# Performance work log

Measured on AMD Instinct MI355X. Metric: run time of the kernel, lower is better.

The kernel has to match this reference:

```python
import jax, jax.numpy as jnp
import numpy as np

NUM_CLASSES = 22
CLIP_LENGTH = 256.0
OVERLAP_THRESH = 0.5
EPS = 1.1920929e-07  # torch.finfo(float32).eps
BOUNDS_LO = jnp.array([0., 15., 30., 60., 96., 256.], dtype=jnp.float32)
BOUNDS_HI = jnp.array([30., 60., 120., 240., 768., 768.], dtype=jnp.float32)


def setup_inputs() -> dict:
    key = jax.random.key(0)
    ks = jax.random.split(key, 9)
    B, K, C, N = 8, 100000, NUM_CLASSES, 32
    loc_data = jax.random.uniform(ks[0], (B, K, 2), jnp.float32)
    conf_data = jax.random.normal(ks[1], (B, K, C), jnp.float32)
    prop_loc_data = jax.random.uniform(ks[2], (B, K, 2), jnp.float32)
    prop_conf_data = jax.random.normal(ks[3], (B, K, C), jnp.float32)
    center_data = jax.random.normal(ks[4], (B, K, 1), jnp.float32)
    # priors: [K,2] = (center in [0,1], pyramid-level index 0..5)
    centers = (jnp.arange(K, dtype=jnp.float32) + 0.5) / K
    levels = jax.random.randint(ks[5], (K,), 0, 6).astype(jnp.float32)
    priors = jnp.stack([centers, levels], axis=-1)
    # targets: [B,N,3] = (start, end, label), label in 1..C-1
    starts = jax.random.uniform(ks[6], (B, N), jnp.float32, 0.0, 0.8)
    lens = jax.random.uniform(ks[7], (B, N), jnp.float32, 0.02, 0.3)
    ends = jnp.clip(starts + lens, 0.0, 1.0)
    labels = jax.random.randint(ks[8], (B, N), 1, C).astype(jnp.float32)
    targets = jnp.stack([starts, ends, labels], axis=-1)
    return {"loc_data": loc_data, "conf_data": conf_data,
            "prop_loc_data": prop_loc_data, "prop_conf_data": prop_conf_data,
            "center_data": center_data, "priors": priors, "targets": targets}


def _calc_iou(pred, tgt):
    # pred/tgt: [..., 2] = (left, right) distances; 1-D segment IoU
    inter = jnp.minimum(pred[..., 0], tgt[..., 0]) + jnp.minimum(pred[..., 1], tgt[..., 1])
    union = pred[..., 0] + pred[..., 1] + tgt[..., 0] + tgt[..., 1] - inter
    return inter / jnp.maximum(union, EPS)


def _giou_elem(pred, tgt):
    inter = jnp.minimum(pred[..., 0], tgt[..., 0]) + jnp.minimum(pred[..., 1], tgt[..., 1])
    union = pred[..., 0] + pred[..., 1] + tgt[..., 0] + tgt[..., 1] - inter
    ious = inter / jnp.maximum(union, EPS)
    ac = jnp.maximum(pred[..., 0], tgt[..., 0]) + jnp.maximum(pred[..., 1], tgt[..., 1])
    gious = ious - (ac - union) / jnp.maximum(ac, EPS)
    return 1.0 - gious


def _focal_sum(logits, tgt):
    # FocalLoss_Ori: softmax probs, pt = p[target]+1e-10, alpha[0]=0.25, alpha[1:]=0.75,
    # loss = -alpha_t * (1-pt)^2 * log(pt), summed over anchors -> [B]
    probs = jax.nn.softmax(logits, axis=-1)
    pt = jnp.take_along_axis(probs, tgt[..., None], axis=-1)[..., 0] + 1e-10
    alpha_t = jnp.where(tgt == 0, 0.25, 0.75)
    return (-alpha_t * (1.0 - pt) ** 2 * jnp.log(pt)).sum(axis=1)


def _forward(loc_data, conf_data, prop_loc_data, prop_conf_data, center_data, priors, targets):
    B, K, C = conf_data.shape
    maxn = 2.0 * CLIP_LENGTH

    def match():  # torch.no_grad() block
        center = priors[:, 0]                              # [K]
        lvl = priors[:, 1].astype(jnp.int32)
        lb = BOUNDS_LO[lvl][None, :, None]                 # [1,K,1]
        rb = BOUNDS_HI[lvl][None, :, None]
        ts, te = targets[..., 0], targets[..., 1]          # [B,N]
        left = (center[None, :, None] - ts[:, None, :]) * CLIP_LENGTH   # [B,K,N]
        right = (te[:, None, :] - center[None, :, None]) * CLIP_LENGTH
        max_dis = jnp.maximum(left, right)
        area = left + right
        bad = (left < 0) | (right < 0) | (max_dis <= lb) | (max_dis > rb)
        area = jnp.where(bad, maxn, area)
        best_area = area.min(axis=2)                       # [B,K]
        best_idx = area.argmin(axis=2)                     # [B,K]
        gs = jnp.take_along_axis(ts, best_idx, axis=1)
        ge = jnp.take_along_axis(te, best_idx, axis=1)
        loc_t = jnp.stack([(center[None, :] - gs) * CLIP_LENGTH,
                           (ge - center[None, :]) * CLIP_LENGTH], axis=-1)  # [B,K,2]
        labels = targets[..., 2]
        conf = jnp.take_along_axis(labels, best_idx, axis=1).astype(jnp.int32)
        conf = jnp.where(best_area >= maxn, 0, conf)
        iou = _calc_iou(loc_data, loc_t)                   # [B,K]
        pos = conf > 0
        has_pos = pos.any(axis=1)
        max_iou = jnp.where(has_pos, jnp.where(pos, iou, -jnp.inf).max(axis=1), 2.0)
        thr = jnp.minimum(OVERLAP_THRESH, max_iou)[:, None]
        prop_conf = jnp.where(iou < thr, 0, conf)
        prop_w = loc_data[..., 0] + loc_data[..., 1]
        prop_loc_t = (loc_t - loc_data) / (0.5 * prop_w[..., None])
        return loc_t, conf, prop_conf, prop_loc_t

    loc_t, conf_t, prop_conf_t, prop_loc_t = jax.lax.stop_gradient(match())
    pos = conf_t > 0                                       # [B,K]
    prop_pos = prop_conf_t > 0
    Nb = jnp.maximum(pos.sum(axis=1), 1).astype(jnp.float32)
    PNb = jnp.maximum(prop_pos.sum(axis=1), 1).astype(jnp.float32)

    # loc giou loss over positives
    loss_l = jnp.where(pos, _giou_elem(loc_data, loc_t), 0.0).sum(axis=1) / Nb

    # prop smooth_l1 over prop positives (beta=1)
    d = jnp.abs(prop_loc_data - prop_loc_t)
    sl1 = jnp.where(d < 1.0, 0.5 * d * d, d - 0.5).sum(axis=-1)   # [B,K]
    loss_prop_l = jnp.where(prop_pos, sl1, 0.0).sum(axis=1) / PNb

    # centerness BCE-with-logits vs refined IoU over positives
    prop_w = loc_data[..., 0] + loc_data[..., 1]
    cur_loc_p = 0.5 * prop_w[..., None] * prop_loc_data + loc_data
    ious_c = jnp.maximum(_calc_iou(cur_loc_p, loc_t), 0.0)
    x = center_data[..., 0]
    bce = jax.nn.softplus(x) - x * ious_c                  # BCEWithLogits(x, y)
    loss_ct = jnp.where(pos, bce, 0.0).sum(axis=1) / Nb

    # focal classification losses over ALL anchors
    loss_c = _focal_sum(conf_data, conf_t) / Nb
    loss_prop_c = _focal_sum(prop_conf_data, prop_conf_t) / PNb

    return jnp.stack([loss_l.mean(), loss_c.mean(), loss_prop_l.mean(),
                      loss_prop_c.mean(), loss_ct.mean()])


def reference(loc_data, conf_data, prop_loc_data, prop_conf_data, center_data, priors, targets):
    return _forward(loc_data, conf_data, prop_loc_data, prop_conf_data,
                    center_data, priors, targets)
```

## Files before the change

kernel.cpp:

```cpp
#include <hip/hip_runtime.h>
#include <math.h>
#include <stdint.h>

#define BLK 256
#define NCLS 22
#define ROWB 88
#define WROWS 32
#define CHB (WROWS * ROWB)
#define CH2 (CHB / 8)
#define EPSF 1.1920929e-07f
#define K1CHUNK (BLK * 4)
#define NB1MAX 128

__device__ __constant__ float c_lo[6] = {0.f, 15.f, 30.f, 60.f, 96.f, 256.f};
__device__ __constant__ float c_hi[6] = {30.f, 60.f, 120.f, 240.f, 768.f, 768.f};

struct MatchRes { float t0, t1; int conf; };

template <int NN>
__device__ __forceinline__ MatchRes do_match_u(float center, int lvl, const float* tg) {
    float lb = c_lo[lvl], rb = c_hi[lvl];
    float best = 1e30f; int bidx = 0;
#pragma unroll
    for (int j = 0; j < NN; ++j) {
        float ts = tg[3 * j], te = tg[3 * j + 1];
        float left  = (center - ts) * 256.f;
        float right = (te - center) * 256.f;
        float md   = fmaxf(left, right);
        float area = left + right;
        bool bad = (left < 0.f) | (right < 0.f) | (md <= lb) | (md > rb);
        area = bad ? 512.f : area;
        if (area < best) { best = area; bidx = j; }
    }
    MatchRes r;
    float gs = tg[3 * bidx], ge = tg[3 * bidx + 1];
    r.t0 = (center - gs) * 256.f;
    r.t1 = (ge - center) * 256.f;
    r.conf = (best >= 512.f) ? 0 : (int)tg[3 * bidx + 2];
    return r;
}

__device__ __forceinline__ MatchRes do_match_d(float center, int lvl, const float* tg, int N) {
    float lb = c_lo[lvl], rb = c_hi[lvl];
    float best = 1e30f; int bidx = 0;
    for (int j = 0; j < N; ++j) {
        float ts = tg[3 * j], te = tg[3 * j + 1];
        float left  = (center - ts) * 256.f;
        float right = (te - center) * 256.f;
        float md   = fmaxf(left, right);
        float area = left + right;
        bool bad = (left < 0.f) | (right < 0.f) | (md <= lb) | (md > rb);
        area = bad ? 512.f : area;
        if (area < best) { best = area; bidx = j; }
    }
    MatchRes r;
    float gs = tg[3 * bidx], ge = tg[3 * bidx + 1];
    r.t0 = (center - gs) * 256.f;
    r.t1 = (ge - center) * 256.f;
    r.conf = (best >= 512.f) ? 0 : (int)tg[3 * bidx + 2];
    return r;
}

__device__ __forceinline__ float calc_iou(float px, float py, float t0, float t1) {
    float inter = fminf(px, t0) + fminf(py, t1);
    float uni = px + py + t0 + t1 - inter;
    return inter / fmaxf(uni, EPSF);
}

__device__ __forceinline__ float focal22_lds(const float2* r2, int tgt) {
    float v[NCLS];
#pragma unroll
    for (int i = 0; i < NCLS / 2; ++i) { float2 x = r2[i]; v[2 * i] = x.x; v[2 * i + 1] = x.y; }
    float m0 = v[0], m1 = v[1], m2 = v[2], m3 = v[3];
#pragma unroll
    for (int i = 4; i < NCLS; i += 4) {
        m0 = fmaxf(m0, v[i]);
        m1 = fmaxf(m1, v[i + 1]);
        if (i + 2 < NCLS) m2 = fmaxf(m2, v[i + 2]);
        if (i + 3 < NCLS) m3 = fmaxf(m3, v[i + 3]);
    }
    float m = fmaxf(fmaxf(m0, m1), fmaxf(m2, m3));
    float sA = 0.f, sB = 0.f, eA = 0.f, eB = 0.f;
#pragma unroll
    for (int i = 0; i < NCLS; i += 2) {
        float ea = __expf(v[i] - m);
        float eb = __expf(v[i + 1] - m);
        sA += ea; sB += eb;
        eA += (i == tgt) ? ea : 0.f;
        eB += (i + 1 == tgt) ? eb : 0.f;
    }
    float pt = (eA + eB) / (sA + sB) + 1e-10f;
    float aa = (tgt == 0) ? 0.25f : 0.75f;
    float om = 1.f - pt;
    return -aa * om * om * __logf(pt);
}

__global__ __launch_bounds__(BLK) void k1_match(const float* __restrict__ loc,
                                                const float* __restrict__ priors,
                                                const float* __restrict__ targets,
                                                float* __restrict__ wsmax,
                                                int K, int N) {
    int b = blockIdx.y;
    __shared__ float tg[96];
    __shared__ float red[4];
    if (threadIdx.x < 3 * N) tg[threadIdx.x] = targets[b * 3 * N + threadIdx.x];
    __syncthreads();
    float my = -INFINITY;
    for (int base = blockIdx.x * K1CHUNK; base < K; base += gridDim.x * K1CHUNK) {
        for (int it = 0; it < 2; ++it) {
            int k0 = base + it * (BLK * 2) + threadIdx.x * 2;
            if (k0 < K) {
                size_t idx = (size_t)b * K + k0;
                float4 pr = reinterpret_cast<const float4*>(priors)[k0 >> 1];
                float4 lp = reinterpret_cast<const float4*>(loc)[idx >> 1];
                MatchRes r0 = (N == 32) ? do_match_u<32>(pr.x, (int)pr.y, tg)
                                        : do_match_d(pr.x, (int)pr.y, tg, N);
                MatchRes r1 = (N == 32) ? do_match_u<32>(pr.z, (int)pr.w, tg)
                                        : do_match_d(pr.z, (int)pr.w, tg, N);
                if (r0.conf > 0) my = fmaxf(my, calc_iou(lp.x, lp.y, r0.t0, r0.t1));
                if (((k0 + 1) < K) && r1.conf > 0)
                    my = fmaxf(my, calc_iou(lp.z, lp.w, r1.t0, r1.t1));
            }
        }
    }
#pragma unroll
    for (int off = 32; off; off >>= 1) my = fmaxf(my, __shfl_xor(my, off));
    int wid = threadIdx.x >> 6;
    if ((threadIdx.x & 63) == 0) red[wid] = my;
    __syncthreads();
    if (threadIdx.x == 0)
        wsmax[b * gridDim.x + blockIdx.x] =
            fmaxf(fmaxf(red[0], red[1]), fmaxf(red[2], red[3]));
}

template <bool UN32>
__global__ __launch_bounds__(BLK) void k2_loss(const float* __restrict__ loc,
                                               const float* __restrict__ conf,
                                               const float* __restrict__ ploc,
                                               const float* __restrict__ pconf,
                                               const float* __restrict__ cent,
                                               const float* __restrict__ priors,
                                               const float* __restrict__ targets,
                                               const float* __restrict__ wsmax,
                                               float* __restrict__ wspart,
                                               int K, int N, int nb1) {
    int b = blockIdx.y;
    int wid = threadIdx.x >> 6, lane = threadIdx.x & 63;
    __shared__ float tg[96];
    __shared__ float red[7][4];
    __shared__ __align__(16) float2 stage[4][2 * CH2];
    if (threadIdx.x < 3 * N) tg[threadIdx.x] = targets[b * 3 * N + threadIdx.x];
    __syncthreads();

    int rb = blockIdx.x * (4 * WROWS) + wid * WROWS;
    int rloc = lane >> 1;
    int r = rb + rloc;
    bool odd = lane & 1;
    bool act = r < K;
    int rc = act ? r : (K - 1);
    size_t idx = (size_t)b * K + rc;

    const float* xybase = odd ? ploc : loc;
    float2 xy = reinterpret_cast<const float2*>(xybase)[idx];
    float ccv = cent[idx];
    float2 pr = reinterpret_cast<const float2*>(priors)[rc];
    float w0 = (lane < nb1) ? wsmax[b * nb1 + lane] : -INFINITY;
    float w1 = (lane + 64 < nb1) ? wsmax[b * nb1 + lane + 64] : -INFINITY;

    float4 cr[3], qr[3];
    {
        const uint8_t* cg = (const uint8_t*)conf;
        const uint8_t* qg = (const uint8_t*)pconf;
        size_t cbase = ((size_t)b * K + (size_t)(rb < K ? rb : 0)) * ROWB;
        size_t endB = ((size_t)(b + 1) * K) * ROWB - 16;
#pragma unroll
        for (int i = 0; i < 3; ++i) {
            size_t so = cbase + (size_t)i * 1024 + (size_t)lane * 16;
            if (so > endB) so = endB;
            cr[i] = *reinterpret_cast<const float4*>(cg + so);
        }
#pragma unroll
        for (int i = 0; i < 3; ++i) {
            size_t so = cbase + (size_t)i * 1024 + (size_t)lane * 16;
            if (so > endB) so = endB;
            qr[i] = *reinterpret_cast<const float4*>(qg + so);
        }
    }

    float mx = fmaxf(w0, w1);
#pragma unroll
    for (int off = 32; off; off >>= 1) mx = fmaxf(mx, __shfl_xor(mx, off));
    float thr = (mx == -INFINITY) ? 0.5f : fminf(0.5f, mx);

    MatchRes mr = UN32 ? do_match_u<32>(pr.x, (int)pr.y, tg)
                       : do_match_d(pr.x, (int)pr.y, tg, N);
    int cf = mr.conf;
    float t0 = mr.t0, t1 = mr.t1;

    float ox = __shfl_xor(xy.x, 1), oy = __shfl_xor(xy.y, 1);
    float lpx = odd ? ox : xy.x, lpy = odd ? oy : xy.y;
    float ppx = odd ? xy.x : ox, ppy = odd ? xy.y : oy;

    float iou = calc_iou(lpx, lpy, t0, t1);
    int pc = (iou < thr) ? 0 : cf;
    float pw = lpx + lpy;

    float s_giou = 0.f, s_sl1 = 0.f, s_bce = 0.f, c_pos = 0.f, c_ppos = 0.f;
    if (!odd && act && cf > 0) {
        c_pos = 1.f;
        float inter = fminf(lpx, t0) + fminf(lpy, t1);
        float uni = lpx + lpy + t0 + t1 - inter;
        float ac = fmaxf(lpx, t0) + fmaxf(lpy, t1);
        float g = iou - (ac - uni) / fmaxf(ac, EPSF);
        s_giou = 1.f - g;
        float cl0 = 0.5f * pw * ppx + lpx;
        float cl1 = 0.5f * pw * ppy + lpy;
        float i2 = fminf(cl0, t0) + fminf(cl1, t1);
        float u2 = cl0 + cl1 + t0 + t1 - i2;
        float iouc = fmaxf(i2 / fmaxf(u2, EPSF), 0.f);
        float sp = fmaxf(ccv, 0.f) + log1pf(__expf(-fabsf(ccv)));
        s_bce = sp - ccv * iouc;
    }
    if (odd && act && pc > 0) {
        c_ppos = 1.f;
        float hpw = 0.5f * pw;
        float plt0 = (t0 - lpx) / hpw;
        float plt1 = (t1 - lpy) / hpw;
        float d0 = fabsf(ppx - plt0), d1 = fabsf(ppy - plt1);
        float f0 = (d0 < 1.f) ? 0.5f * d0 * d0 : d0 - 0.5f;
        float f1 = (d1 < 1.f) ? 0.5f * d1 * d1 : d1 - 0.5f;
        s_sl1 = f0 + f1;
    }

    {
        float2* sb = stage[wid];
#pragma unroll
        for (int i = 0; i < 3; ++i) {
            int e2 = i * 128 + lane * 2;
            if (e2 < CH2) {
                sb[e2]     = make_float2(cr[i].x, cr[i].y);
                sb[e2 + 1] = make_float2(cr[i].z, cr[i].w);
            }
        }
#pragma unroll
        for (int i = 0; i < 3; ++i) {
            int e2 = i * 128 + lane * 2;
            if (e2 < CH2) {
                sb[CH2 + e2]     = make_float2(qr[i].x, qr[i].y);
                sb[CH2 + e2 + 1] = make_float2(qr[i].z, qr[i].w);
            }
        }
    }
    asm volatile("s_waitcnt lgkmcnt(0)" ::: "memory");

    const float2* rowp = stage[wid] + (odd ? CH2 : 0) + rloc * (ROWB / 8);
    int ftgt = odd ? pc : cf;
    float f = act ? focal22_lds(rowp, ftgt) : 0.f;
    float s_fc  = odd ? 0.f : f;
    float s_fpc = odd ? f : 0.f;

#pragma unroll
    for (int off = 32; off; off >>= 1) {
        s_giou += __shfl_xor(s_giou, off);
        s_sl1  += __shfl_xor(s_sl1, off);
        s_bce  += __shfl_xor(s_bce, off);
        s_fc   += __shfl_xor(s_fc, off);
        s_fpc  += __shfl_xor(s_fpc, off);
        c_pos  += __shfl_xor(c_pos, off);
        c_ppos += __shfl_xor(c_ppos, off);
    }
    if ((threadIdx.x & 63) == 0) {
        red[0][wid] = s_giou; red[1][wid] = s_sl1; red[2][wid] = s_bce;
        red[3][wid] = s_fc;   red[4][wid] = s_fpc; red[5][wid] = c_pos;
        red[6][wid] = c_ppos;
    }
    __syncthreads();
    if (threadIdx.x < 7) {
        float v = red[threadIdx.x][0] + red[threadIdx.x][1] +
                  red[threadIdx.x][2] + red[threadIdx.x][3];
        wspart[((size_t)b * gridDim.x + blockIdx.x) * 8 + threadIdx.x] = v;
    }
}

__global__ __launch_bounds__(512) void k3_final(const float* __restrict__ wspart,
                                                float* __restrict__ out, int B, int nb2) {
    int w = threadIdx.x >> 6, lane = threadIdx.x & 63;
    __shared__ float ls[8][5];
    float s[7] = {0.f, 0.f, 0.f, 0.f, 0.f, 0.f, 0.f};
    if (w < B) {
        for (int e = lane; e < nb2; e += 64) {
            const float* a = wspart + ((size_t)w * nb2 + e) * 8;
#pragma unroll
            for (int i = 0; i < 7; ++i) s[i] += a[i];
        }
    }
#pragma unroll
    for (int off = 32; off; off >>= 1)
#pragma unroll
        for (int i = 0; i < 7; ++i) s[i] += __shfl_xor(s[i], off);
    if (w < B && lane == 0) {
        float Nb  = fmaxf(s[5], 1.f);
        float PNb = fmaxf(s[6], 1.f);
        ls[w][0] = s[0] / Nb;
        ls[w][1] = s[3] / Nb;
        ls[w][2] = s[1] / PNb;
        ls[w][3] = s[4] / PNb;
        ls[w][4] = s[2] / Nb;
    }
    __syncthreads();
    if (threadIdx.x < 5) {
        float tt = 0.f;
        for (int bb = 0; bb < B; ++bb) tt += ls[bb][threadIdx.x];
        out[threadIdx.x] = tt / (float)B;
    }
}

extern "C" void kernel_launch(void* const* d_in, const int* in_sizes, int n_in,
                              void* d_out, int out_size, void* d_ws, size_t ws_size,
                              hipStream_t stream) {
    const float* loc     = (const float*)d_in[0];
    const float* conf    = (const float*)d_in[1];
    const float* ploc    = (const float*)d_in[2];
    const float* pconf   = (const float*)d_in[3];
    const float* cent    = (const float*)d_in[4];
    const float* priors  = (const float*)d_in[5];
    const float* targets = (const float*)d_in[6];
    int K = in_sizes[5] / 2;
    int B = in_sizes[0] / (2 * K);
    int N = in_sizes[6] / (3 * B);

    float* wsmax  = (float*)d_ws;
    float* wspart = (float*)d_ws + 1024;
    float* out = (float*)d_out;

    int nb1 = (K + K1CHUNK - 1) / K1CHUNK;
    if (nb1 > NB1MAX) nb1 = NB1MAX;
    int rows_per_blk = 4 * WROWS;
    int nb2 = (K + rows_per_blk - 1) / rows_per_blk;

    k1_match<<<dim3(nb1, B), dim3(BLK), 0, stream>>>(loc, priors, targets, wsmax, K, N);
    if (N == 32)
        k2_loss<true><<<dim3(nb2, B), dim3(BLK), 0, stream>>>(
            loc, conf, ploc, pconf, cent, priors, targets, wsmax, wspart, K, N, nb1);
    else
        k2_loss<false><<<dim3(nb2, B), dim3(BLK), 0, stream>>>(
            loc, conf, ploc, pconf, cent, priors, targets, wsmax, wspart, K, N, nb1);
    k3_final<<<dim3(1), dim3(512), 0, stream>>>(wspart, out, B, nb2);
}
```

Before: 66.99 us.

## Process four row chunks per wave with double-buffered conf loads and lane-dense matching

```diff
diff --git a/kernel.cpp b/kernel.cpp
--- a/kernel.cpp
+++ b/kernel.cpp
@@ -6,8 +6,10 @@
 #define NCLS 22
 #define ROWB 88
 #define WROWS 32
-#define CHB (WROWS * ROWB)
-#define CH2 (CHB / 8)
+#define CPW 4
+#define RPW (WROWS * CPW)
+#define RPB (RPW * 4)
+#define CH2 352
 #define EPSF 1.1920929e-07f
 #define K1CHUNK (BLK * 4)
 #define NB1MAX 128
@@ -67,29 +69,27 @@
     return inter / fmaxf(uni, EPSF);
 }
 
+__device__ __forceinline__ float fmax3(float a, float b, float c) {
+    return fmaxf(fmaxf(a, b), c);
+}
+
 __device__ __forceinline__ float focal22_lds(const float2* r2, int tgt) {
     float v[NCLS];
 #pragma unroll
     for (int i = 0; i < NCLS / 2; ++i) { float2 x = r2[i]; v[2 * i] = x.x; v[2 * i + 1] = x.y; }
-    float m0 = v[0], m1 = v[1], m2 = v[2], m3 = v[3];
-#pragma unroll
-    for (int i = 4; i < NCLS; i += 4) {
-        m0 = fmaxf(m0, v[i]);
-        m1 = fmaxf(m1, v[i + 1]);
-        if (i + 2 < NCLS) m2 = fmaxf(m2, v[i + 2]);
-        if (i + 3 < NCLS) m3 = fmaxf(m3, v[i + 3]);
-    }
-    float m = fmaxf(fmaxf(m0, m1), fmaxf(m2, m3));
-    float sA = 0.f, sB = 0.f, eA = 0.f, eB = 0.f;
+    float xt = reinterpret_cast<const float*>(r2)[tgt];
+    float a0 = fmax3(v[0], v[1], v[2]),  a1 = fmax3(v[3], v[4], v[5]);
+    float a2 = fmax3(v[6], v[7], v[8]),  a3 = fmax3(v[9], v[10], v[11]);
+    float a4 = fmax3(v[12], v[13], v[14]), a5 = fmax3(v[15], v[16], v[17]);
+    float a6 = fmax3(v[18], v[19], v[20]);
+    float m = fmax3(fmax3(a0, a1, a2), fmax3(a3, a4, a5), fmaxf(a6, v[21]));
+    float sA = 0.f, sB = 0.f;
 #pragma unroll
     for (int i = 0; i < NCLS; i += 2) {
-        float ea = __expf(v[i] - m);
-        float eb = __expf(v[i + 1] - m);
-        sA += ea; sB += eb;
-        eA += (i == tgt) ? ea : 0.f;
-        eB += (i + 1 == tgt) ? eb : 0.f;
-    }
-    float pt = (eA + eB) / (sA + sB) + 1e-10f;
+        sA += __expf(v[i] - m);
+        sB += __expf(v[i + 1] - m);
+    }
+    float pt = __expf(xt - m) / (sA + sB) + 1e-10f;
     float aa = (tgt == 0) ? 0.25f : 0.75f;
     float om = 1.f - pt;
     return -aa * om * om * __logf(pt);
@@ -149,115 +149,130 @@
     __shared__ float tg[96];
     __shared__ float red[7][4];
     __shared__ __align__(16) float2 stage[4][2 * CH2];
+    __shared__ float2 msct[4][RPW];
+    __shared__ float  mscf[4][RPW];
     if (threadIdx.x < 3 * N) tg[threadIdx.x] = targets[b * 3 * N + threadIdx.x];
     __syncthreads();
 
-    int rb = blockIdx.x * (4 * WROWS) + wid * WROWS;
+    int rb = blockIdx.x * RPB + wid * RPW;
+    bool odd = lane & 1;
     int rloc = lane >> 1;
-    int r = rb + rloc;
-    bool odd = lane & 1;
-    bool act = r < K;
-    int rc = act ? r : (K - 1);
-    size_t idx = (size_t)b * K + rc;
-
-    const float* xybase = odd ? ploc : loc;
-    float2 xy = reinterpret_cast<const float2*>(xybase)[idx];
-    float ccv = cent[idx];
-    float2 pr = reinterpret_cast<const float2*>(priors)[rc];
+
     float w0 = (lane < nb1) ? wsmax[b * nb1 + lane] : -INFINITY;
     float w1 = (lane + 64 < nb1) ? wsmax[b * nb1 + lane + 64] : -INFINITY;
-
-    float4 cr[3], qr[3];
-    {
-        const uint8_t* cg = (const uint8_t*)conf;
-        const uint8_t* qg = (const uint8_t*)pconf;
-        size_t cbase = ((size_t)b * K + (size_t)(rb < K ? rb : 0)) * ROWB;
-        size_t endB = ((size_t)(b + 1) * K) * ROWB - 16;
-#pragma unroll
-        for (int i = 0; i < 3; ++i) {
-            size_t so = cbase + (size_t)i * 1024 + (size_t)lane * 16;
-            if (so > endB) so = endB;
-            cr[i] = *reinterpret_cast<const float4*>(cg + so);
-        }
-#pragma unroll
-        for (int i = 0; i < 3; ++i) {
-            size_t so = cbase + (size_t)i * 1024 + (size_t)lane * 16;
-            if (so > endB) so = endB;
-            qr[i] = *reinterpret_cast<const float4*>(qg + so);
-        }
-    }
-
     float mx = fmaxf(w0, w1);
 #pragma unroll
     for (int off = 32; off; off >>= 1) mx = fmaxf(mx, __shfl_xor(mx, off));
     float thr = (mx == -INFINITY) ? 0.5f : fminf(0.5f, mx);
 
-    MatchRes mr = UN32 ? do_match_u<32>(pr.x, (int)pr.y, tg)
-                       : do_match_d(pr.x, (int)pr.y, tg, N);
-    int cf = mr.conf;
-    float t0 = mr.t0, t1 = mr.t1;
-
-    float ox = __shfl_xor(xy.x, 1), oy = __shfl_xor(xy.y, 1);
-    float lpx = odd ? ox : xy.x, lpy = odd ? oy : xy.y;
-    float ppx = odd ? xy.x : ox, ppy = odd ? xy.y : oy;
-
-    float iou = calc_iou(lpx, lpy, t0, t1);
-    int pc = (iou < thr) ? 0 : cf;
-    float pw = lpx + lpy;
-
-    float s_giou = 0.f, s_sl1 = 0.f, s_bce = 0.f, c_pos = 0.f, c_ppos = 0.f;
-    if (!odd && act && cf > 0) {
-        c_pos = 1.f;
-        float inter = fminf(lpx, t0) + fminf(lpy, t1);
-        float uni = lpx + lpy + t0 + t1 - inter;
-        float ac = fmaxf(lpx, t0) + fmaxf(lpy, t1);
-        float g = iou - (ac - uni) / fmaxf(ac, EPSF);
-        s_giou = 1.f - g;
-        float cl0 = 0.5f * pw * ppx + lpx;
-        float cl1 = 0.5f * pw * ppy + lpy;
-        float i2 = fminf(cl0, t0) + fminf(cl1, t1);
-        float u2 = cl0 + cl1 + t0 + t1 - i2;
-        float iouc = fmaxf(i2 / fmaxf(u2, EPSF), 0.f);
-        float sp = fmaxf(ccv, 0.f) + log1pf(__expf(-fabsf(ccv)));
-        s_bce = sp - ccv * iouc;
-    }
-    if (odd && act && pc > 0) {
-        c_ppos = 1.f;
-        float hpw = 0.5f * pw;
-        float plt0 = (t0 - lpx) / hpw;
-        float plt1 = (t1 - lpy) / hpw;
-        float d0 = fabsf(ppx - plt0), d1 = fabsf(ppy - plt1);
-        float f0 = (d0 < 1.f) ? 0.5f * d0 * d0 : d0 - 0.5f;
-        float f1 = (d1 < 1.f) ? 0.5f * d1 * d1 : d1 - 0.5f;
-        s_sl1 = f0 + f1;
-    }
-
-    {
-        float2* sb = stage[wid];
-#pragma unroll
-        for (int i = 0; i < 3; ++i) {
-            int e2 = i * 128 + lane * 2;
-            if (e2 < CH2) {
-                sb[e2]     = make_float2(cr[i].x, cr[i].y);
-                sb[e2 + 1] = make_float2(cr[i].z, cr[i].w);
-            }
+#pragma unroll
+    for (int h = 0; h < 2; ++h) {
+        int r = rb + h * 64 + lane;
+        int rc = (r < K) ? r : (K - 1);
+        float2 pr = reinterpret_cast<const float2*>(priors)[rc];
+        MatchRes mr = UN32 ? do_match_u<32>(pr.x, (int)pr.y, tg)
+                           : do_match_d(pr.x, (int)pr.y, tg, N);
+        msct[wid][h * 64 + lane] = make_float2(mr.t0, mr.t1);
+        mscf[wid][h * 64 + lane] = (float)mr.conf;
+    }
+
+    const uint8_t* cg = (const uint8_t*)conf;
+    const uint8_t* qg = (const uint8_t*)pconf;
+    size_t endB = ((size_t)(b + 1) * K) * ROWB - 16;
+
+    float4 cA[3], qA[3], cB[3], qB[3];
+#define LOADC(c, cd, qd) {                                                        \
+    size_t cb = ((size_t)b * K + (size_t)(rb + (c) * WROWS)) * ROWB;              \
+    _Pragma("unroll") for (int i = 0; i < 3; ++i) {                               \
+        size_t so = cb + (size_t)i * 1024 + (size_t)lane * 16;                    \
+        if (so > endB) so = endB;                                                 \
+        cd[i] = *reinterpret_cast<const float4*>(cg + so); }                      \
+    _Pragma("unroll") for (int i = 0; i < 3; ++i) {                               \
+        size_t so = cb + (size_t)i * 1024 + (size_t)lane * 16;                    \
+        if (so > endB) so = endB;                                                 \
+        qd[i] = *reinterpret_cast<const float4*>(qg + so); } }
+
+#define STOREC(cd, qd) {                                                          \
+    float2* sb = stage[wid];                                                      \
+    _Pragma("unroll") for (int i = 0; i < 3; ++i) {                               \
+        int e2 = i * 128 + lane * 2;                                              \
+        if (e2 < CH2) {                                                           \
+            sb[e2]     = make_float2(cd[i].x, cd[i].y);                           \
+            sb[e2 + 1] = make_float2(cd[i].z, cd[i].w); } }                       \
+    _Pragma("unroll") for (int i = 0; i < 3; ++i) {                               \
+        int e2 = i * 128 + lane * 2;                                              \
+        if (e2 < CH2) {                                                           \
+            sb[CH2 + e2]     = make_float2(qd[i].x, qd[i].y);                     \
+            sb[CH2 + e2 + 1] = make_float2(qd[i].z, qd[i].w); } } }
+
+    LOADC(0, cA, qA)
+
+    float s_giou = 0.f, s_sl1 = 0.f, s_bce = 0.f, s_fc = 0.f, s_fpc = 0.f,
+          c_pos = 0.f, c_ppos = 0.f;
+
+#pragma unroll
+    for (int c = 0; c < CPW; ++c) {
+        if (c == 0)      { LOADC(1, cB, qB) }
+        else if (c == 1) { LOADC(2, cA, qA) }
+        else if (c == 2) { LOADC(3, cB, qB) }
+
+        int rl = c * WROWS + rloc;
+        int r = rb + rl;
+        bool act = r < K;
+        int rc = act ? r : (K - 1);
+        size_t idx = (size_t)b * K + rc;
+        const float* xyb = odd ? ploc : loc;
+        float2 xy = reinterpret_cast<const float2*>(xyb)[idx];
+        float ccv = odd ? 0.f : cent[idx];
+
+        if (c & 1) { STOREC(cB, qB) } else { STOREC(cA, qA) }
+        asm volatile("s_waitcnt lgkmcnt(0)" ::: "memory");
+
+        float2 mt = msct[wid][rl];
+        int cf = (int)mscf[wid][rl];
+        float t0 = mt.x, t1 = mt.y;
+
+        float ox = __shfl_xor(xy.x, 1), oy = __shfl_xor(xy.y, 1);
+        float lpx = odd ? ox : xy.x, lpy = odd ? oy : xy.y;
+        float ppx = odd ? xy.x : ox, ppy = odd ? xy.y : oy;
+
+        float iou = calc_iou(lpx, lpy, t0, t1);
+        int pc = (iou < thr) ? 0 : cf;
+        float pw = lpx + lpy;
+
+        if (!odd && act && cf > 0) {
+            c_pos += 1.f;
+            float inter = fminf(lpx, t0) + fminf(lpy, t1);
+            float uni = lpx + lpy + t0 + t1 - inter;
+            float ac = fmaxf(lpx, t0) + fmaxf(lpy, t1);
+            float g = iou - (ac - uni) / fmaxf(ac, EPSF);
+            s_giou += 1.f - g;
+            float cl0 = 0.5f * pw * ppx + lpx;
+            float cl1 = 0.5f * pw * ppy + lpy;
+            float i2 = fminf(cl0, t0) + fminf(cl1, t1);
+            float u2 = cl0 + cl1 + t0 + t1 - i2;
+            float iouc = fmaxf(i2 / fmaxf(u2, EPSF), 0.f);
+            float sp = fmaxf(ccv, 0.f) + log1pf(__expf(-fabsf(ccv)));
+            s_bce += sp - ccv * iouc;
         }
-#pragma unroll
-        for (int i = 0; i < 3; ++i) {
-            int e2 = i * 128 + lane * 2;
-            if (e2 < CH2) {
-                sb[CH2 + e2]     = make_float2(qr[i].x, qr[i].y);
-                sb[CH2 + e2 + 1] = make_float2(qr[i].z, qr[i].w);
-            }
+        if (odd && act && pc > 0) {
+            c_ppos += 1.f;
+            float hpw = 0.5f * pw;
+            float plt0 = (t0 - lpx) / hpw;
+            float plt1 = (t1 - lpy) / hpw;
+            float d0 = fabsf(ppx - plt0), d1 = fabsf(ppy - plt1);
+            float f0 = (d0 < 1.f) ? 0.5f * d0 * d0 : d0 - 0.5f;
+            float f1 = (d1 < 1.f) ? 0.5f * d1 * d1 : d1 - 0.5f;
+            s_sl1 += f0 + f1;
         }
-    }
-    asm volatile("s_waitcnt lgkmcnt(0)" ::: "memory");
-
-    const float2* rowp = stage[wid] + (odd ? CH2 : 0) + rloc * (ROWB / 8);
-    int ftgt = odd ? pc : cf;
-    float f = act ? focal22_lds(rowp, ftgt) : 0.f;
-    float s_fc  = odd ? 0.f : f;
-    float s_fpc = odd ? f : 0.f;
+
+        const float2* rowp = stage[wid] + (odd ? CH2 : 0) + rloc * (ROWB / 8);
+        int ftgt = odd ? pc : cf;
+        float f = act ? focal22_lds(rowp, ftgt) : 0.f;
+        if (odd) s_fpc += f; else s_fc += f;
+    }
+#undef LOADC
+#undef STOREC
 
 #pragma unroll
     for (int off = 32; off; off >>= 1) {
@@ -335,8 +350,7 @@
 
     int nb1 = (K + K1CHUNK - 1) / K1CHUNK;
     if (nb1 > NB1MAX) nb1 = NB1MAX;
-    int rows_per_blk = 4 * WROWS;
-    int nb2 = (K + rows_per_blk - 1) / rows_per_blk;
+    int nb2 = (K + RPB - 1) / RPB;
 
     k1_match<<<dim3(nb1, B), dim3(BLK), 0, stream>>>(loc, priors, targets, wsmax, K, N);
     if (N == 32)
```

New measurement: 62.42 us. -6.8%, faster.

## Cache per-anchor match results from match kernel and reuse in loss kernel

Applied to the files above, without the earlier changes.

```diff
diff --git a/kernel.cpp b/kernel.cpp
--- a/kernel.cpp
+++ b/kernel.cpp
@@ -6,11 +6,11 @@
 #define NCLS 22
 #define ROWB 88
 #define WROWS 32
-#define CHB (WROWS * ROWB)
-#define CH2 (CHB / 8)
+#define RPB (4 * WROWS)
+#define CH2 352
 #define EPSF 1.1920929e-07f
-#define K1CHUNK (BLK * 4)
-#define NB1MAX 128
+#define K1PAIRS 2
+#define K1CHUNK (BLK * 2 * K1PAIRS)
 
 __device__ __constant__ float c_lo[6] = {0.f, 15.f, 30.f, 60.f, 96.f, 256.f};
 __device__ __constant__ float c_hi[6] = {30.f, 60.f, 120.f, 240.f, 768.f, 768.f};
@@ -67,29 +67,27 @@
     return inter / fmaxf(uni, EPSF);
 }
 
+__device__ __forceinline__ float fmax3(float a, float b, float c) {
+    return fmaxf(fmaxf(a, b), c);
+}
+
 __device__ __forceinline__ float focal22_lds(const float2* r2, int tgt) {
     float v[NCLS];
 #pragma unroll
     for (int i = 0; i < NCLS / 2; ++i) { float2 x = r2[i]; v[2 * i] = x.x; v[2 * i + 1] = x.y; }
-    float m0 = v[0], m1 = v[1], m2 = v[2], m3 = v[3];
-#pragma unroll
-    for (int i = 4; i < NCLS; i += 4) {
-        m0 = fmaxf(m0, v[i]);
-        m1 = fmaxf(m1, v[i + 1]);
-        if (i + 2 < NCLS) m2 = fmaxf(m2, v[i + 2]);
-        if (i + 3 < NCLS) m3 = fmaxf(m3, v[i + 3]);
-    }
-    float m = fmaxf(fmaxf(m0, m1), fmaxf(m2, m3));
-    float sA = 0.f, sB = 0.f, eA = 0.f, eB = 0.f;
+    float xt = reinterpret_cast<const float*>(r2)[tgt];
+    float a0 = fmax3(v[0], v[1], v[2]),   a1 = fmax3(v[3], v[4], v[5]);
+    float a2 = fmax3(v[6], v[7], v[8]),   a3 = fmax3(v[9], v[10], v[11]);
+    float a4 = fmax3(v[12], v[13], v[14]), a5 = fmax3(v[15], v[16], v[17]);
+    float a6 = fmax3(v[18], v[19], v[20]);
+    float m = fmax3(fmax3(a0, a1, a2), fmax3(a3, a4, a5), fmaxf(a6, v[21]));
+    float sA = 0.f, sB = 0.f;
 #pragma unroll
     for (int i = 0; i < NCLS; i += 2) {
-        float ea = __expf(v[i] - m);
-        float eb = __expf(v[i + 1] - m);
-        sA += ea; sB += eb;
-        eA += (i == tgt) ? ea : 0.f;
-        eB += (i + 1 == tgt) ? eb : 0.f;
-    }
-    float pt = (eA + eB) / (sA + sB) + 1e-10f;
+        sA += __expf(v[i] - m);
+        sB += __expf(v[i + 1] - m);
+    }
+    float pt = __expf(xt - m) / (sA + sB) + 1e-10f;
     float aa = (tgt == 0) ? 0.25f : 0.75f;
     float om = 1.f - pt;
     return -aa * om * om * __logf(pt);
@@ -99,27 +97,33 @@
                                                 const float* __restrict__ priors,
                                                 const float* __restrict__ targets,
                                                 float* __restrict__ wsmax,
+                                                float4* __restrict__ wsmatch,
                                                 int K, int N) {
     int b = blockIdx.y;
+    int chunk0 = blockIdx.x * K1CHUNK;
     __shared__ float tg[96];
     __shared__ float red[4];
     if (threadIdx.x < 3 * N) tg[threadIdx.x] = targets[b * 3 * N + threadIdx.x];
     __syncthreads();
     float my = -INFINITY;
-    for (int base = blockIdx.x * K1CHUNK; base < K; base += gridDim.x * K1CHUNK) {
-        for (int it = 0; it < 2; ++it) {
-            int k0 = base + it * (BLK * 2) + threadIdx.x * 2;
-            if (k0 < K) {
-                size_t idx = (size_t)b * K + k0;
-                float4 pr = reinterpret_cast<const float4*>(priors)[k0 >> 1];
-                float4 lp = reinterpret_cast<const float4*>(loc)[idx >> 1];
-                MatchRes r0 = (N == 32) ? do_match_u<32>(pr.x, (int)pr.y, tg)
-                                        : do_match_d(pr.x, (int)pr.y, tg, N);
-                MatchRes r1 = (N == 32) ? do_match_u<32>(pr.z, (int)pr.w, tg)
-                                        : do_match_d(pr.z, (int)pr.w, tg, N);
-                if (r0.conf > 0) my = fmaxf(my, calc_iou(lp.x, lp.y, r0.t0, r0.t1));
-                if (((k0 + 1) < K) && r1.conf > 0)
-                    my = fmaxf(my, calc_iou(lp.z, lp.w, r1.t0, r1.t1));
+    for (int it = 0; it < K1PAIRS; ++it) {
+        int k0 = chunk0 + it * (BLK * 2) + threadIdx.x * 2;
+        if (k0 < K) {
+            size_t idx = (size_t)b * K + k0;
+            float4 pr = reinterpret_cast<const float4*>(priors)[k0 >> 1];
+            float4 lp = reinterpret_cast<const float4*>(loc)[idx >> 1];
+            MatchRes r0 = (N == 32) ? do_match_u<32>(pr.x, (int)pr.y, tg)
+                                    : do_match_d(pr.x, (int)pr.y, tg, N);
+            MatchRes r1 = (N == 32) ? do_match_u<32>(pr.z, (int)pr.w, tg)
+                                    : do_match_d(pr.z, (int)pr.w, tg, N);
+            float i0 = calc_iou(lp.x, lp.y, r0.t0, r0.t1);
+            float i1 = calc_iou(lp.z, lp.w, r1.t0, r1.t1);
+            bool ok1 = (k0 + 1) < K;
+            if (r0.conf > 0) my = fmaxf(my, i0);
+            if (ok1 && r1.conf > 0) my = fmaxf(my, i1);
+            if (wsmatch) {
+                wsmatch[idx] = make_float4(r0.t0, r0.t1, (float)r0.conf, i0);
+                if (ok1) wsmatch[idx + 1] = make_float4(r1.t0, r1.t1, (float)r1.conf, i1);
             }
         }
     }
@@ -133,7 +137,7 @@
             fmaxf(fmaxf(red[0], red[1]), fmaxf(red[2], red[3]));
 }
 
-template <bool UN32>
+template <bool PREM>
 __global__ __launch_bounds__(BLK) void k2_loss(const float* __restrict__ loc,
                                                const float* __restrict__ conf,
                                                const float* __restrict__ ploc,
@@ -142,6 +146,7 @@
                                                const float* __restrict__ priors,
                                                const float* __restrict__ targets,
                                                const float* __restrict__ wsmax,
+                                               const float4* __restrict__ wsmatch,
                                                float* __restrict__ wspart,
                                                int K, int N, int nb1) {
     int b = blockIdx.y;
@@ -149,10 +154,12 @@
     __shared__ float tg[96];
     __shared__ float red[7][4];
     __shared__ __align__(16) float2 stage[4][2 * CH2];
-    if (threadIdx.x < 3 * N) tg[threadIdx.x] = targets[b * 3 * N + threadIdx.x];
-    __syncthreads();
-
-    int rb = blockIdx.x * (4 * WROWS) + wid * WROWS;
+    if (!PREM) {
+        if (threadIdx.x < 3 * N) tg[threadIdx.x] = targets[b * 3 * N + threadIdx.x];
+        __syncthreads();
+    }
+
+    int rb = blockIdx.x * RPB + wid * WROWS;
     int rloc = lane >> 1;
     int r = rb + rloc;
     bool odd = lane & 1;
@@ -160,12 +167,13 @@
     int rc = act ? r : (K - 1);
     size_t idx = (size_t)b * K + rc;
 
+    float w0 = (lane < nb1) ? wsmax[b * nb1 + lane] : -INFINITY;
+    float w1 = (lane + 64 < nb1) ? wsmax[b * nb1 + lane + 64] : -INFINITY;
+    float4 m4;
+    if (PREM) m4 = wsmatch[idx];
     const float* xybase = odd ? ploc : loc;
     float2 xy = reinterpret_cast<const float2*>(xybase)[idx];
     float ccv = cent[idx];
-    float2 pr = reinterpret_cast<const float2*>(priors)[rc];
-    float w0 = (lane < nb1) ? wsmax[b * nb1 + lane] : -INFINITY;
-    float w1 = (lane + 64 < nb1) ? wsmax[b * nb1 + lane + 64] : -INFINITY;
 
     float4 cr[3], qr[3];
     {
@@ -192,16 +200,21 @@
     for (int off = 32; off; off >>= 1) mx = fmaxf(mx, __shfl_xor(mx, off));
     float thr = (mx == -INFINITY) ? 0.5f : fminf(0.5f, mx);
 
-    MatchRes mr = UN32 ? do_match_u<32>(pr.x, (int)pr.y, tg)
-                       : do_match_d(pr.x, (int)pr.y, tg, N);
-    int cf = mr.conf;
-    float t0 = mr.t0, t1 = mr.t1;
+    float t0, t1; int cf;
+    if (PREM) {
+        t0 = m4.x; t1 = m4.y; cf = (int)m4.z;
+    } else {
+        float2 pr = reinterpret_cast<const float2*>(priors)[rc];
+        MatchRes mr = (N == 32) ? do_match_u<32>(pr.x, (int)pr.y, tg)
+                                : do_match_d(pr.x, (int)pr.y, tg, N);
+        t0 = mr.t0; t1 = mr.t1; cf = mr.conf;
+    }
 
     float ox = __shfl_xor(xy.x, 1), oy = __shfl_xor(xy.y, 1);
     float lpx = odd ? ox : xy.x, lpy = odd ? oy : xy.y;
     float ppx = odd ? xy.x : ox, ppy = odd ? xy.y : oy;
 
-    float iou = calc_iou(lpx, lpy, t0, t1);
+    float iou = PREM ? m4.w : calc_iou(lpx, lpy, t0, t1);
     int pc = (iou < thr) ? 0 : cf;
     float pw = lpx + lpy;
 
@@ -331,19 +344,24 @@
 
     float* wsmax  = (float*)d_ws;
     float* wspart = (float*)d_ws + 1024;
+    const size_t match_off = (size_t)1 << 20;
+    float4* wsmatch = (float4*)((char*)d_ws + match_off);
     float* out = (float*)d_out;
 
     int nb1 = (K + K1CHUNK - 1) / K1CHUNK;
-    if (nb1 > NB1MAX) nb1 = NB1MAX;
-    int rows_per_blk = 4 * WROWS;
-    int nb2 = (K + rows_per_blk - 1) / rows_per_blk;
-
-    k1_match<<<dim3(nb1, B), dim3(BLK), 0, stream>>>(loc, priors, targets, wsmax, K, N);
-    if (N == 32)
+    int nb2 = (K + RPB - 1) / RPB;
+
+    bool prem = (ws_size >= match_off + (size_t)B * K * 16) &&
+                ((size_t)(1024 + B * nb2 * 8) * 4 <= match_off) &&
+                (K % 2 == 0) && (nb1 <= 128);
+
+    k1_match<<<dim3(nb1, B), dim3(BLK), 0, stream>>>(loc, priors, targets, wsmax,
+                                                     prem ? wsmatch : nullptr, K, N);
+    if (prem)
         k2_loss<true><<<dim3(nb2, B), dim3(BLK), 0, stream>>>(
-            loc, conf, ploc, pconf, cent, priors, targets, wsmax, wspart, K, N, nb1);
+            loc, conf, ploc, pconf, cent, priors, targets, wsmax, wsmatch, wspart, K, N, nb1);
     else
         k2_loss<false><<<dim3(nb2, B), dim3(BLK), 0, stream>>>(
-            loc, conf, ploc, pconf, cent, priors, targets, wsmax, wspart, K, N, nb1);
+            loc, conf, ploc, pconf, cent, priors, targets, wsmax, wsmatch, wspart, K, N, nb1);
     k3_final<<<dim3(1), dim3(512), 0, stream>>>(wspart, out, B, nb2);
 }
```

Result: faster. 58.07 us (-13.3%).
